# Optimization experiments

Hardware: AMD Instinct MI355X
Metric: run time of the kernel (lower is better)

Reference implementation:

```python
import jax, jax.numpy as jnp
import numpy as np

N_CTRL_U = 64
N_CTRL_V = 64
N_EVAL = 2001  # int(1/0.0005) + 1


def _clamped_knots(p, n_ctrl, dtype):
    """Clamped uniform knot vector on [0,1], length n_ctrl + p + 1."""
    n_internal = n_ctrl - p - 1
    internal = jnp.linspace(0.0, 1.0, n_internal + 2, dtype=dtype)[1:-1]
    return jnp.concatenate([
        jnp.zeros(p + 1, dtype=dtype), internal, jnp.ones(p + 1, dtype=dtype)
    ])


def _find_spans(knots, u, p, n_ctrl):
    """Knot-span index for each parameter (NURBS book A2.1, via searchsorted)."""
    return jnp.clip(jnp.searchsorted(knots, u, side='right') - 1, p, n_ctrl - 1)


def _basis_functions(knots, spans, u, p):
    """Cox-de-Boor nonzero basis functions (NURBS book A2.2), vectorized over u.
    Returns [N, p+1]."""
    Ns = [jnp.ones_like(u)]
    left = {}
    right = {}
    for j in range(1, p + 1):
        left[j] = u - knots[spans + 1 - j]
        right[j] = knots[spans + j] - u
        saved = jnp.zeros_like(u)
        new = []
        for r in range(j):
            temp = Ns[r] / (right[r + 1] + left[j - r])
            new.append(saved + right[r + 1] * temp)
            saved = left[j - r] * temp
        new.append(saved)
        Ns = new
    return jnp.stack(Ns, axis=-1)


def setup_inputs() -> dict:
    key = jax.random.key(0)
    k1, = jax.random.split(key, 1)
    control_points = jax.random.normal(k1, (N_CTRL_U, N_CTRL_V, 3), dtype=jnp.float32)
    params_u = jnp.linspace(0.0, 1.0, N_EVAL, dtype=jnp.float32)
    params_v = jnp.linspace(0.0, 1.0, N_EVAL, dtype=jnp.float32)
    return {"control_points": control_points, "params_u": params_u,
            "params_v": params_v, "degree": 3}


def reference(control_points, params_u, params_v, degree):
    p = int(degree)
    n_u, n_v, d = control_points.shape
    dt = control_points.dtype
    ku = _clamped_knots(p, n_u, dt)
    kv = _clamped_knots(p, n_v, dt)
    su = _find_spans(ku, params_u, p, n_u)          # [Nu]
    sv = _find_spans(kv, params_v, p, n_v)          # [Nv]
    Bu = _basis_functions(ku, su, params_u, p)      # [Nu, p+1]
    Bv = _basis_functions(kv, sv, params_v, p)      # [Nv, p+1]
    off = jnp.arange(p + 1)
    iu = su[:, None] - p + off[None, :]             # [Nu, p+1]
    iv = sv[:, None] - p + off[None, :]             # [Nv, p+1]
    # Contract u first to keep intermediates small: [Nu, p+1, n_v, d] -> [Nu, n_v, d]
    ctrl_u = control_points[iu]                     # gather rows by span
    curve_u = jnp.einsum('ua,uavd->uvd', Bu, ctrl_u)
    # Gather v spans then contract: [Nu, Nv, p+1, d] -> [Nu, Nv, d]
    pts = curve_u[:, iv]
    return jnp.einsum('vb,uvbd->uvd', Bv, pts)
```

## Files before the change

### kernel.cpp

```cpp
#include <hip/hip_runtime.h>

#define N_EVAL 2001
#define NCTRL  64

__device__ __forceinline__ float knotv(int i) {
    if (i <= 3) return 0.0f;
    if (i >= NCTRL) return 1.0f;
    return (float)(i - 3) * (1.0f / 61.0f);
}

__device__ __forceinline__ void basis_p3(float u, int& span, float4& N) {
    int s = 3 + (int)floorf(u * 61.0f);
    s = max(3, min(63, s));
    while (s < 63 && knotv(s + 1) <= u) ++s;
    while (s > 3 && knotv(s) > u) --s;

    float left[4], right[4], Ns[4];
    Ns[0] = 1.0f;
    #pragma unroll
    for (int j = 1; j <= 3; ++j) {
        left[j]  = u - knotv(s + 1 - j);
        right[j] = knotv(s + j) - u;
        float saved = 0.0f;
        #pragma unroll
        for (int r = 0; r < j; ++r) {
            float temp = Ns[r] / (right[r + 1] + left[j - r]);
            Ns[r] = saved + right[r + 1] * temp;
            saved = left[j - r] * temp;
        }
        Ns[j] = saved;
    }
    span = s;
    N = make_float4(Ns[0], Ns[1], Ns[2], Ns[3]);
}

__global__ void basis_kernel(const float* __restrict__ pu, const float* __restrict__ pv,
                             float4* __restrict__ Bu, float4* __restrict__ Bv,
                             int* __restrict__ su, int* __restrict__ sv) {
    int gid = blockIdx.x * blockDim.x + threadIdx.x;
    if (gid < 2048) {
        if (gid < N_EVAL) {
            int s; float4 N;
            basis_p3(pu[gid], s, N);
            Bu[gid] = N; su[gid] = s;
        }
    } else {
        int i = gid - 2048;
        if (i < N_EVAL) {
            int s; float4 N;
            basis_p3(pv[i], s, N);
            Bv[i] = N; sv[i] = s;
        }
    }
}

__global__ __launch_bounds__(256) void eval_kernel(const float* __restrict__ cp,
                                                   const float4* __restrict__ Bu,
                                                   const float4* __restrict__ Bv,
                                                   const int* __restrict__ su,
                                                   const int* __restrict__ sv,
                                                   float* __restrict__ out) {
    __shared__ float4 lds4[NCTRL];
    const int u = blockIdx.y;
    const int t = threadIdx.x;
    const int s_u = su[u];
    const float4 bu = Bu[u];

    if (t < NCTRL * 3) {
        const int base = (s_u - 3) * (NCTRL * 3);
        float c = bu.x * cp[base +       t]
                + bu.y * cp[base + 192 + t]
                + bu.z * cp[base + 384 + t]
                + bu.w * cp[base + 576 + t];
        int j = t / 3, d = t - 3 * j;
        ((float*)lds4)[j * 4 + d] = c;
    }
    __syncthreads();

    const int v = blockIdx.x * 256 + t;
    if (v >= N_EVAL) return;
    const float4 bv = Bv[v];
    const int iv0 = sv[v] - 3;
    float4 c0 = lds4[iv0 + 0];
    float4 c1 = lds4[iv0 + 1];
    float4 c2 = lds4[iv0 + 2];
    float4 c3 = lds4[iv0 + 3];
    float x = bv.x * c0.x + bv.y * c1.x + bv.z * c2.x + bv.w * c3.x;
    float y = bv.x * c0.y + bv.y * c1.y + bv.z * c2.y + bv.w * c3.y;
    float z = bv.x * c0.z + bv.y * c1.z + bv.z * c2.z + bv.w * c3.z;

    size_t o = ((size_t)u * N_EVAL + v) * 3;
    out[o + 0] = x;
    out[o + 1] = y;
    out[o + 2] = z;
}

extern "C" void kernel_launch(void* const* d_in, const int* in_sizes, int n_in,
                              void* d_out, int out_size, void* d_ws, size_t ws_size,
                              hipStream_t stream) {
    const float* cp = (const float*)d_in[0];
    const float* pu = (const float*)d_in[1];
    const float* pv = (const float*)d_in[2];
    float* out = (float*)d_out;

    float4* Bu = (float4*)d_ws;
    float4* Bv = Bu + 2048;
    int* su = (int*)(Bu + 4096);
    int* sv = su + 2048;

    basis_kernel<<<16, 256, 0, stream>>>(pu, pv, Bu, Bv, su, sv);

    dim3 grid((N_EVAL + 255) / 256, N_EVAL);
    eval_kernel<<<grid, 256, 0, stream>>>(cp, Bu, Bv, su, sv, out);
}
```

Before: 83.95 us.

## Process full output row per block and coalesce stores via LDS staging

Each block now handles one u row and loops over all v in chunks of 256. The curve contraction is computed once per row instead of once per 256-wide tile. Results are staged in shared memory so the stride-3 xyz writes go out as contiguous coalesced stores. This adds barriers per chunk and gives fewer, longer-running blocks, in exchange for less redundant control-point work and better store coalescing.

```diff
diff --git a/kernel.cpp b/kernel.cpp
--- a/kernel.cpp
+++ b/kernel.cpp
@@ -60,8 +60,10 @@
                                                    const int* __restrict__ su,
                                                    const int* __restrict__ sv,
                                                    float* __restrict__ out) {
-    __shared__ float4 lds4[NCTRL];
-    const int u = blockIdx.y;
+    __shared__ float4 curve[NCTRL];
+    __shared__ float  stage[768];
+
+    const int u = blockIdx.x;
     const int t = threadIdx.x;
     const int s_u = su[u];
     const float4 bu = Bu[u];
@@ -73,26 +75,42 @@
                 + bu.z * cp[base + 384 + t]
                 + bu.w * cp[base + 576 + t];
         int j = t / 3, d = t - 3 * j;
-        ((float*)lds4)[j * 4 + d] = c;
+        ((float*)curve)[j * 4 + d] = c;
     }
     __syncthreads();
 
-    const int v = blockIdx.x * 256 + t;
-    if (v >= N_EVAL) return;
-    const float4 bv = Bv[v];
-    const int iv0 = sv[v] - 3;
-    float4 c0 = lds4[iv0 + 0];
-    float4 c1 = lds4[iv0 + 1];
-    float4 c2 = lds4[iv0 + 2];
-    float4 c3 = lds4[iv0 + 3];
-    float x = bv.x * c0.x + bv.y * c1.x + bv.z * c2.x + bv.w * c3.x;
-    float y = bv.x * c0.y + bv.y * c1.y + bv.z * c2.y + bv.w * c3.y;
-    float z = bv.x * c0.z + bv.y * c1.z + bv.z * c2.z + bv.w * c3.z;
+    float* orow = out + (size_t)u * (N_EVAL * 3);
 
-    size_t o = ((size_t)u * N_EVAL + v) * 3;
-    out[o + 0] = x;
-    out[o + 1] = y;
-    out[o + 2] = z;
+    #pragma unroll
+    for (int k = 0; k < 8; ++k) {
+        const int v = k * 256 + t;
+        float x = 0.f, y = 0.f, z = 0.f;
+        if (v < N_EVAL) {
+            const float4 bv = Bv[v];
+            const int iv0 = sv[v] - 3;
+            float4 c0 = curve[iv0 + 0];
+            float4 c1 = curve[iv0 + 1];
+            float4 c2 = curve[iv0 + 2];
+            float4 c3 = curve[iv0 + 3];
+            x = bv.x * c0.x + bv.y * c1.x + bv.z * c2.x + bv.w * c3.x;
+            y = bv.x * c0.y + bv.y * c1.y + bv.z * c2.y + bv.w * c3.y;
+            z = bv.x * c0.z + bv.y * c1.z + bv.z * c2.z + bv.w * c3.z;
+        }
+        if (k) __syncthreads();
+        if (v < N_EVAL) {
+            stage[3 * t + 0] = x;
+            stage[3 * t + 1] = y;
+            stage[3 * t + 2] = z;
+        }
+        __syncthreads();
+        const int rowbase = k * 768;
+        #pragma unroll
+        for (int j = 0; j < 3; ++j) {
+            int idx = j * 256 + t;
+            if (rowbase + idx < N_EVAL * 3)
+                orow[rowbase + idx] = stage[idx];
+        }
+    }
 }
 
 extern "C" void kernel_launch(void* const* d_in, const int* in_sizes, int n_in,
@@ -109,7 +127,5 @@
     int* sv = su + 2048;
 
     basis_kernel<<<16, 256, 0, stream>>>(pu, pv, Bu, Bv, su, sv);
-
-    dim3 grid((N_EVAL + 255) / 256, N_EVAL);
-    eval_kernel<<<grid, 256, 0, stream>>>(cp, Bu, Bv, su, sv, out);
+    eval_kernel<<<N_EVAL, 256, 0, stream>>>(cp, Bu, Bv, su, sv, out);
 }
```

Measured after the change: 83.05 us. Within noise of the previous version (-1.1%).
